# Kernel optimization log

Hardware: AMD Instinct MI355X
Metric: run time of the kernel (lower is better)

The kernel has to match this reference:

```python
import jax, jax.numpy as jnp
import numpy as np

G, NPG, DEG = 64, 1024, 16          # graphs, nodes/graph, avg degree
N, E = G * NPG, G * NPG * DEG        # 65536 nodes, 1048576 edges
F, H = 128, 128                      # num_features, n_hidden
K1, K2 = NPG // 2, NPG // 4          # ceil(0.5*1024)=512, ceil(0.5*512)=256


def setup_inputs() -> dict:
    key = jax.random.key(0)
    ks = jax.random.split(key, 16)
    x = jax.random.normal(ks[0], (N, F), dtype=jnp.float32)
    # edges constrained within each graph (block-diagonal adjacency)
    offs = (jnp.arange(G, dtype=jnp.int32) * NPG)[:, None]
    src = (jax.random.randint(ks[1], (G, E // G), 0, NPG, dtype=jnp.int32) + offs).reshape(-1)
    dst = (jax.random.randint(ks[2], (G, E // G), 0, NPG, dtype=jnp.int32) + offs).reshape(-1)
    def lin(k, fi, fo):
        s = 1.0 / np.sqrt(fi)
        return jax.random.uniform(k, (fi, fo), jnp.float32, -s, s)
    return dict(
        x=x, src=src, dst=dst,
        W1=lin(ks[3], F, H),  b1=jnp.zeros((H,), jnp.float32),
        Ws1=lin(ks[4], H, 1), bs1=jnp.zeros((1,), jnp.float32),
        W2=lin(ks[5], H, H),  b2=jnp.zeros((H,), jnp.float32),
        Ws2=lin(ks[6], H, 1), bs2=jnp.zeros((1,), jnp.float32),
        Wl1=lin(ks[7], 2 * H, H), bl1=jnp.zeros((H,), jnp.float32),
        Wl2=lin(ks[8], H, 1),     bl2=jnp.zeros((1,), jnp.float32),
    )


def gcn_conv(x, src, dst, ew, W, b):
    """GCNConv: D^-1/2 (A+I) D^-1/2 (x W) + b, with edge weights ew."""
    n = x.shape[0]
    h = x @ W
    loop = jnp.arange(n, dtype=src.dtype)
    s = jnp.concatenate([src, loop])
    d = jnp.concatenate([dst, loop])
    w = jnp.concatenate([ew, jnp.ones((n,), x.dtype)])
    deg = jax.ops.segment_sum(w, d, num_segments=n)
    dinv = jnp.where(deg > 0, jax.lax.rsqrt(jnp.maximum(deg, 1e-12)), 0.0)
    norm = dinv[s] * dinv[d] * w
    return jax.ops.segment_sum(norm[:, None] * h[s], d, num_segments=n) + b


def sag_pool(x, src, dst, ew, Ws, bs, n_per_graph, k):
    """SAGPooling: GCN attention score, per-graph top-k, x*tanh(score), edge prune via mask."""
    n = x.shape[0]
    g = n // n_per_graph
    score = gcn_conv(x, src, dst, ew, Ws, bs)[:, 0]                 # [n]
    _, idx = jax.lax.top_k(score.reshape(g, n_per_graph), k)        # [g, k]
    perm = (idx + (jnp.arange(g, dtype=jnp.int32) * n_per_graph)[:, None]).reshape(-1)
    xn = x[perm] * jnp.tanh(score[perm])[:, None]                   # [g*k, H]
    kept = jnp.zeros((n,), bool).at[perm].set(True)
    nmap = jnp.zeros((n,), jnp.int32).at[perm].set(jnp.arange(g * k, dtype=jnp.int32))
    valid = kept[src] & kept[dst] & (ew > 0)
    ewn = jnp.where(valid, ew, 0.0)
    srcn = jnp.where(valid, nmap[src], 0)
    dstn = jnp.where(valid, nmap[dst], 0)
    return xn, srcn, dstn, ewn


def reference(x, src, dst, W1, b1, Ws1, bs1, W2, b2, Ws2, bs2, Wl1, bl1, Wl2, bl2):
    ew = jnp.ones((src.shape[0],), x.dtype)
    h = jax.nn.relu(gcn_conv(x, src, dst, ew, W1, b1))
    h, s1, d1, ew1 = sag_pool(h, src, dst, ew, Ws1, bs1, NPG, K1)
    hb = h.reshape(G, K1, H)
    x1 = jnp.concatenate([hb.max(axis=1), hb.mean(axis=1)], axis=1)  # [G, 2H]
    h = jax.nn.relu(gcn_conv(h, s1, d1, ew1, W2, b2))
    h, s2, d2, ew2 = sag_pool(h, s1, d1, ew1, Ws2, bs2, K1, K2)
    hb = h.reshape(G, K2, H)
    x2 = jnp.concatenate([hb.max(axis=1), hb.mean(axis=1)], axis=1)
    z = x1 + x2
    z = jax.nn.relu(z @ Wl1 + bl1)                                  # dropout: eval mode (identity)
    return (z @ Wl2 + bl2)[:, 0]                                     # [G]
```

## Files before the change

kernel.cpp:

```cpp
#include <hip/hip_runtime.h>
#include <math.h>

constexpr int NN1 = 65536;
constexpr int EE  = 1048576;
constexpr int GG  = 64;
constexpr int HH  = 128;
constexpr int NPG = 1024;
constexpr int EPG = 16384;
constexpr int K1  = 512;
constexpr int M1  = GG * K1;
constexpr int K2  = 256;
constexpr int M2  = GG * K2;

__device__ __forceinline__ int xcd_swz(int bid, int nblk)
{
    return (bid & 7) * (nblk >> 3) + (bid >> 3);
}

__device__ __forceinline__ float4 f4add(float4 a, float4 b)
{
    a.x += b.x; a.y += b.y; a.z += b.z; a.w += b.w; return a;
}

__global__ __launch_bounds__(256) void gemm1_k(const float* __restrict__ A,
                                               const float* __restrict__ W,
                                               const int* __restrict__ rbeg,
                                               const int* __restrict__ rend,
                                               float* __restrict__ C)
{
    __shared__ float Wl[64 * 160];
    const int t    = threadIdx.x;
    const int rowg = t >> 3;
    const int cg   = t & 7;
    const int b    = xcd_swz(blockIdx.x, gridDim.x);
    const int r0   = (b << 7) + rowg;

    const float* Ar0 = A + ((size_t)r0 << 7);
    const float* Ar1 = Ar0 + (32 << 7);
    const float* Ar2 = Ar1 + (32 << 7);
    const float* Ar3 = Ar2 + (32 << 7);

    float acc[4][16];
#pragma unroll
    for (int i = 0; i < 4; ++i)
#pragma unroll
        for (int j = 0; j < 16; ++j) acc[i][j] = 0.f;

    {
        const float4* Wg = (const float4*)W;
#pragma unroll
        for (int i = 0; i < 8; ++i) {
            int idx = t + (i << 8);
            int k   = idx >> 5;
            int c4  = (idx & 31) << 2;
            *(float4*)&Wl[k * 160 + (c4 >> 4) * 20 + (c4 & 15)] = Wg[idx];
        }
    }
    float4 xc0 = *(const float4*)(Ar0), xc1 = *(const float4*)(Ar1);
    float4 xc2 = *(const float4*)(Ar2), xc3 = *(const float4*)(Ar3);
    __syncthreads();

    const float* wbase = &Wl[cg * 20];

#pragma unroll 1
    for (int k0 = 0; k0 < 64; k0 += 4) {
        float4 xn0 = *(const float4*)(Ar0 + k0 + 4);
        float4 xn1 = *(const float4*)(Ar1 + k0 + 4);
        float4 xn2 = *(const float4*)(Ar2 + k0 + 4);
        float4 xn3 = *(const float4*)(Ar3 + k0 + 4);
#pragma unroll
        for (int kk = 0; kk < 4; ++kk) {
            const float* wr = wbase + (k0 + kk) * 160;
            float x0 = ((const float*)&xc0)[kk], x1 = ((const float*)&xc1)[kk];
            float x2 = ((const float*)&xc2)[kk], x3 = ((const float*)&xc3)[kk];
#pragma unroll
            for (int jh = 0; jh < 16; jh += 8) {
                float wv[8];
                *(float4*)&wv[0] = *(const float4*)(wr + jh);
                *(float4*)&wv[4] = *(const float4*)(wr + jh + 4);
#pragma unroll
                for (int j = 0; j < 8; ++j) {
                    acc[0][jh + j] = fmaf(x0, wv[j], acc[0][jh + j]);
                    acc[1][jh + j] = fmaf(x1, wv[j], acc[1][jh + j]);
                    acc[2][jh + j] = fmaf(x2, wv[j], acc[2][jh + j]);
                    acc[3][jh + j] = fmaf(x3, wv[j], acc[3][jh + j]);
                }
            }
        }
        xc0 = xn0; xc1 = xn1; xc2 = xn2; xc3 = xn3;
    }
    __syncthreads();
    {
        const float4* Wg = (const float4*)(W + 64 * 128);
#pragma unroll
        for (int i = 0; i < 8; ++i) {
            int idx = t + (i << 8);
            int k   = idx >> 5;
            int c4  = (idx & 31) << 2;
            *(float4*)&Wl[k * 160 + (c4 >> 4) * 20 + (c4 & 15)] = Wg[idx];
        }
    }
    __syncthreads();

#pragma unroll 1
    for (int k0 = 64; k0 < 128; k0 += 4) {
        bool pf = (k0 < 124);
        float4 xn0, xn1, xn2, xn3;
        if (pf) {
            xn0 = *(const float4*)(Ar0 + k0 + 4);
            xn1 = *(const float4*)(Ar1 + k0 + 4);
            xn2 = *(const float4*)(Ar2 + k0 + 4);
            xn3 = *(const float4*)(Ar3 + k0 + 4);
        }
#pragma unroll
        for (int kk = 0; kk < 4; ++kk) {
            const float* wr = wbase + (k0 - 64 + kk) * 160;
            float x0 = ((const float*)&xc0)[kk], x1 = ((const float*)&xc1)[kk];
            float x2 = ((const float*)&xc2)[kk], x3 = ((const float*)&xc3)[kk];
#pragma unroll
            for (int jh = 0; jh < 16; jh += 8) {
                float wv[8];
                *(float4*)&wv[0] = *(const float4*)(wr + jh);
                *(float4*)&wv[4] = *(const float4*)(wr + jh + 4);
#pragma unroll
                for (int j = 0; j < 8; ++j) {
                    acc[0][jh + j] = fmaf(x0, wv[j], acc[0][jh + j]);
                    acc[1][jh + j] = fmaf(x1, wv[j], acc[1][jh + j]);
                    acc[2][jh + j] = fmaf(x2, wv[j], acc[2][jh + j]);
                    acc[3][jh + j] = fmaf(x3, wv[j], acc[3][jh + j]);
                }
            }
        }
        if (pf) { xc0 = xn0; xc1 = xn1; xc2 = xn2; xc3 = xn3; }
    }

#pragma unroll
    for (int i = 0; i < 4; ++i) {
        int r = r0 + (i << 5);
        float deg = (float)(rend[r] - rbeg[r]) + 1.0f;
        float sc = 1.0f / sqrtf(deg);
        float* cp = C + ((size_t)r << 7) + (cg << 4);
#pragma unroll
        for (int j = 0; j < 16; j += 4) {
            float4 v;
            v.x = acc[i][j] * sc; v.y = acc[i][j + 1] * sc;
            v.z = acc[i][j + 2] * sc; v.w = acc[i][j + 3] * sc;
            *(float4*)(cp + j) = v;
        }
    }
}

__global__ __launch_bounds__(256) void gemm2_k(const float* __restrict__ A,
                                               const float* __restrict__ W,
                                               const int* __restrict__ rbeg,
                                               const int* __restrict__ rend,
                                               const int* __restrict__ perm,
                                               const float* __restrict__ tsel,
                                               float* __restrict__ C)
{
    __shared__ float Wl[64 * 160];
    const int t    = threadIdx.x;
    const int rowg = t >> 3;
    const int cg   = t & 7;
    const int b    = xcd_swz(blockIdx.x, gridDim.x);
    const int r0   = (b << 7) + rowg;

    const float* Ar0 = A + ((size_t)perm[r0] << 7);
    const float* Ar1 = A + ((size_t)perm[r0 + 32] << 7);
    const float* Ar2 = A + ((size_t)perm[r0 + 64] << 7);
    const float* Ar3 = A + ((size_t)perm[r0 + 96] << 7);

    float acc[4][16];
#pragma unroll
    for (int i = 0; i < 4; ++i)
#pragma unroll
        for (int j = 0; j < 16; ++j) acc[i][j] = 0.f;

    {
        const float4* Wg = (const float4*)W;
#pragma unroll
        for (int i = 0; i < 8; ++i) {
            int idx = t + (i << 8);
            int k   = idx >> 5;
            int c4  = (idx & 31) << 2;
            *(float4*)&Wl[k * 160 + (c4 >> 4) * 20 + (c4 & 15)] = Wg[idx];
        }
    }
    float4 xc0 = *(const float4*)(Ar0), xc1 = *(const float4*)(Ar1);
    float4 xc2 = *(const float4*)(Ar2), xc3 = *(const float4*)(Ar3);
    __syncthreads();

    const float* wbase = &Wl[cg * 20];

#pragma unroll 1
    for (int k0 = 0; k0 < 64; k0 += 4) {
        float4 xn0 = *(const float4*)(Ar0 + k0 + 4);
        float4 xn1 = *(const float4*)(Ar1 + k0 + 4);
        float4 xn2 = *(const float4*)(Ar2 + k0 + 4);
        float4 xn3 = *(const float4*)(Ar3 + k0 + 4);
#pragma unroll
        for (int kk = 0; kk < 4; ++kk) {
            const float* wr = wbase + (k0 + kk) * 160;
            float x0 = ((const float*)&xc0)[kk], x1 = ((const float*)&xc1)[kk];
            float x2 = ((const float*)&xc2)[kk], x3 = ((const float*)&xc3)[kk];
#pragma unroll
            for (int jh = 0; jh < 16; jh += 8) {
                float wv[8];
                *(float4*)&wv[0] = *(const float4*)(wr + jh);
                *(float4*)&wv[4] = *(const float4*)(wr + jh + 4);
#pragma unroll
                for (int j = 0; j < 8; ++j) {
                    acc[0][jh + j] = fmaf(x0, wv[j], acc[0][jh + j]);
                    acc[1][jh + j] = fmaf(x1, wv[j], acc[1][jh + j]);
                    acc[2][jh + j] = fmaf(x2, wv[j], acc[2][jh + j]);
                    acc[3][jh + j] = fmaf(x3, wv[j], acc[3][jh + j]);
                }
            }
        }
        xc0 = xn0; xc1 = xn1; xc2 = xn2; xc3 = xn3;
    }
    __syncthreads();
    {
        const float4* Wg = (const float4*)(W + 64 * 128);
#pragma unroll
        for (int i = 0; i < 8; ++i) {
            int idx = t + (i << 8);
            int k   = idx >> 5;
            int c4  = (idx & 31) << 2;
            *(float4*)&Wl[k * 160 + (c4 >> 4) * 20 + (c4 & 15)] = Wg[idx];
        }
    }
    __syncthreads();

#pragma unroll 1
    for (int k0 = 64; k0 < 128; k0 += 4) {
        bool pf = (k0 < 124);
        float4 xn0, xn1, xn2, xn3;
        if (pf) {
            xn0 = *(const float4*)(Ar0 + k0 + 4);
            xn1 = *(const float4*)(Ar1 + k0 + 4);
            xn2 = *(const float4*)(Ar2 + k0 + 4);
            xn3 = *(const float4*)(Ar3 + k0 + 4);
        }
#pragma unroll
        for (int kk = 0; kk < 4; ++kk) {
            const float* wr = wbase + (k0 - 64 + kk) * 160;
            float x0 = ((const float*)&xc0)[kk], x1 = ((const float*)&xc1)[kk];
            float x2 = ((const float*)&xc2)[kk], x3 = ((const float*)&xc3)[kk];
#pragma unroll
            for (int jh = 0; jh < 16; jh += 8) {
                float wv[8];
                *(float4*)&wv[0] = *(const float4*)(wr + jh);
                *(float4*)&wv[4] = *(const float4*)(wr + jh + 4);
#pragma unroll
                for (int j = 0; j < 8; ++j) {
                    acc[0][jh + j] = fmaf(x0, wv[j], acc[0][jh + j]);
                    acc[1][jh + j] = fmaf(x1, wv[j], acc[1][jh + j]);
                    acc[2][jh + j] = fmaf(x2, wv[j], acc[2][jh + j]);
                    acc[3][jh + j] = fmaf(x3, wv[j], acc[3][jh + j]);
                }
            }
        }
        if (pf) { xc0 = xn0; xc1 = xn1; xc2 = xn2; xc3 = xn3; }
    }

#pragma unroll
    for (int i = 0; i < 4; ++i) {
        int r = r0 + (i << 5);
        float deg = (float)(rend[r] - rbeg[r]) + 1.0f;
        float sc = tsel[r] / sqrtf(deg);
        float* cp = C + ((size_t)r << 7) + (cg << 4);
#pragma unroll
        for (int j = 0; j < 16; j += 4) {
            float4 v;
            v.x = acc[i][j] * sc; v.y = acc[i][j + 1] * sc;
            v.z = acc[i][j + 2] * sc; v.w = acc[i][j + 3] * sc;
            *(float4*)(cp + j) = v;
        }
    }
}

__global__ __launch_bounds__(1024) void build_csr1_k(const int* __restrict__ src, const int* __restrict__ dst,
                                                     int* __restrict__ rbeg, int* __restrict__ rend,
                                                     int* __restrict__ csr)
{
    __shared__ int cnt[NPG];
    int t = threadIdx.x;
    int g = xcd_swz(blockIdx.x, GG);
    int ebase = g * EPG;
    cnt[t] = 0;
    __syncthreads();
#pragma unroll
    for (int k = 0; k < EPG / 1024; ++k) {
        int d = dst[ebase + t + k * 1024] & (NPG - 1);
        atomicAdd(&cnt[d], 1);
    }
    __syncthreads();
    int deg0 = cnt[t];
    int val = deg0;
    for (int off = 1; off < NPG; off <<= 1) {
        int u = (t >= off) ? cnt[t - off] : 0;
        __syncthreads();
        val += u; cnt[t] = val;
        __syncthreads();
    }
    int node = g * NPG + t;
    rbeg[node] = ebase + val - deg0;
    rend[node] = ebase + val;
    cnt[t] = val - deg0;
    __syncthreads();
#pragma unroll
    for (int k = 0; k < EPG / 1024; ++k) {
        int e = ebase + t + k * 1024;
        int d = dst[e] & (NPG - 1);
        int pos = atomicAdd(&cnt[d], 1);
        csr[ebase + pos] = src[e];
    }
}

__global__ __launch_bounds__(256) void agg_feat_k(const float4* __restrict__ XWs,
                                                  const int* __restrict__ rbeg, const int* __restrict__ rend,
                                                  const int* __restrict__ csr,
                                                  const float* __restrict__ bias, const float* __restrict__ Ws,
                                                  float* __restrict__ hout, float* __restrict__ hss, int n)
{
    int b    = xcd_swz(blockIdx.x, gridDim.x);
    int half = threadIdx.x >> 5;
    int lane = threadIdx.x & 31;
    int node = (b << 3) + half;
    if (node >= n) return;
    const float4* Xf = XWs + lane;

    float4 A = make_float4(0.f, 0.f, 0.f, 0.f), B = A, C = A, D = A;
    int p0 = rbeg[node], p1 = rend[node];
    int p = p0;
    for (; p + 8 <= p1; p += 8) {
        int s0 = csr[p], s1 = csr[p + 1], s2 = csr[p + 2], s3 = csr[p + 3];
        int s4 = csr[p + 4], s5 = csr[p + 5], s6 = csr[p + 6], s7 = csr[p + 7];
        float4 v0 = Xf[(size_t)s0 << 5], v1 = Xf[(size_t)s1 << 5];
        float4 v2 = Xf[(size_t)s2 << 5], v3 = Xf[(size_t)s3 << 5];
        float4 v4 = Xf[(size_t)s4 << 5], v5 = Xf[(size_t)s5 << 5];
        float4 v6 = Xf[(size_t)s6 << 5], v7 = Xf[(size_t)s7 << 5];
        A = f4add(A, v0); B = f4add(B, v1); C = f4add(C, v2); D = f4add(D, v3);
        A = f4add(A, v4); B = f4add(B, v5); C = f4add(C, v6); D = f4add(D, v7);
    }
    for (; p + 4 <= p1; p += 4) {
        int s0 = csr[p], s1 = csr[p + 1], s2 = csr[p + 2], s3 = csr[p + 3];
        float4 v0 = Xf[(size_t)s0 << 5], v1 = Xf[(size_t)s1 << 5];
        float4 v2 = Xf[(size_t)s2 << 5], v3 = Xf[(size_t)s3 << 5];
        A = f4add(A, v0); B = f4add(B, v1); C = f4add(C, v2); D = f4add(D, v3);
    }
    for (; p < p1; ++p) {
        int s = csr[p];
        A = f4add(A, Xf[(size_t)s << 5]);
    }
    float4 acc = f4add(f4add(A, B), f4add(C, D));
    acc = f4add(acc, Xf[(size_t)node << 5]);

    float dd = 1.0f / sqrtf((float)(p1 - p0) + 1.0f);
    float4 bb = *(const float4*)(bias + (lane << 2));
    acc.x = fmaxf(fmaf(acc.x, dd, bb.x), 0.f);
    acc.y = fmaxf(fmaf(acc.y, dd, bb.y), 0.f);
    acc.z = fmaxf(fmaf(acc.z, dd, bb.z), 0.f);
    acc.w = fmaxf(fmaf(acc.w, dd, bb.w), 0.f);
    *(float4*)(hout + ((size_t)node << 7) + (lane << 2)) = acc;

    float4 wsv = *(const float4*)(Ws + (lane << 2));
    float pq = acc.x * wsv.x + acc.y * wsv.y + acc.z * wsv.z + acc.w * wsv.w;
#pragma unroll
    for (int off = 16; off > 0; off >>= 1) pq += __shfl_down(pq, off, 32);
    if (lane == 0) hss[node] = dd * pq;
}

template <int NNE, int KK, bool BUILD>
__global__ void sctopk_k(const int* __restrict__ rbeg, const int* __restrict__ rend,
                         const int* __restrict__ csr, const float* __restrict__ hss,
                         const float* __restrict__ bsp,
                         int* __restrict__ perm, float* __restrict__ tsel,
                         const int* __restrict__ src, const int* __restrict__ dst,
                         int* __restrict__ rbeg2, int* __restrict__ rend2,
                         int* __restrict__ csr2,
                         const float* __restrict__ h, float* __restrict__ xout)
{
    __shared__ unsigned long long keys[NNE];
    __shared__ float hl[NNE];
    __shared__ int   pix[KK];
    __shared__ float tsl[KK];
    int t = threadIdx.x;
    int g = xcd_swz(blockIdx.x, GG);
    int node = g * NNE + t;
    hl[t] = hss[node];
    __syncthreads();

    int p0 = rbeg[node], p1 = rend[node];
    float a = 0.f, b = 0.f, c = 0.f, e = 0.f;
    int p = p0;
    for (; p + 8 <= p1; p += 8) {
        int s0 = csr[p] & (NNE - 1), s1 = csr[p + 1] & (NNE - 1);
        int s2 = csr[p + 2] & (NNE - 1), s3 = csr[p + 3] & (NNE - 1);
        int s4 = csr[p + 4] & (NNE - 1), s5 = csr[p + 5] & (NNE - 1);
        int s6 = csr[p + 6] & (NNE - 1), s7 = csr[p + 7] & (NNE - 1);
        a += hl[s0]; b += hl[s1]; c += hl[s2]; e += hl[s3];
        a += hl[s4]; b += hl[s5]; c += hl[s6]; e += hl[s7];
    }
    for (; p + 4 <= p1; p += 4) {
        int s0 = csr[p] & (NNE - 1), s1 = csr[p + 1] & (NNE - 1);
        int s2 = csr[p + 2] & (NNE - 1), s3 = csr[p + 3] & (NNE - 1);
        a += hl[s0]; b += hl[s1]; c += hl[s2]; e += hl[s3];
    }
    for (; p < p1; ++p) a += hl[csr[p] & (NNE - 1)];
    float dd = 1.0f / sqrtf((float)(p1 - p0) + 1.0f);
    float s = fmaf((a + b) + (c + e) + hl[t], dd, bsp[0]);

    unsigned u = __float_as_uint(s);
    u = (u & 0x80000000u) ? ~u : (u | 0x80000000u);
    __syncthreads();
    keys[t] = (((unsigned long long)u) << 32) | (unsigned)(NNE - 1 - t);
    __syncthreads();
    for (int k = 2; k <= NNE; k <<= 1) {
        for (int j = k >> 1; j > 0; j >>= 1) {
            int ixj = t ^ j;
            if (ixj > t) {
                unsigned long long ka = keys[t], kb = keys[ixj];
                bool up = ((t & k) == 0);
                if ((ka > kb) == up) { keys[t] = kb; keys[ixj] = ka; }
            }
            __syncthreads();
        }
    }
    unsigned long long key = keys[NNE - 1 - t];
    int idx = NNE - 1 - (int)(key & 0xFFFFFFFFu);
    if (t < KK) {
        unsigned uu = (unsigned)(key >> 32);
        float sc = __uint_as_float((uu & 0x80000000u) ? (uu ^ 0x80000000u) : ~uu);
        float tv = tanhf(sc);
        pix[t] = g * NNE + idx;
        tsl[t] = tv;
        if (BUILD) {
            perm[g * KK + t] = g * NNE + idx;
            tsel[g * KK + t] = tv;
        }
    }

    if (BUILD) {
        constexpr int EPT = BUILD ? (EPG / NNE) : 1;
        __syncthreads();
        int* nml = (int*)hl;
        int* cnt = (int*)keys;
        nml[t] = -1;
        if (t < KK) cnt[t] = 0;
        __syncthreads();
        if (t < KK) nml[idx] = t;
        __syncthreads();

        int ebase = g * EPG;
        int nsl[EPT], ndl[EPT];
#pragma unroll
        for (int k = 0; k < EPT; ++k) {
            int e = ebase + t + k * NNE;
            nsl[k] = nml[src[e] & (NNE - 1)];
            ndl[k] = nml[dst[e] & (NNE - 1)];
            if (nsl[k] >= 0 && ndl[k] >= 0) atomicAdd(&cnt[ndl[k]], 1);
        }
        __syncthreads();
        int deg0 = 0, val = 0;
        if (t < KK) { deg0 = cnt[t]; val = deg0; }
        for (int off = 1; off < KK; off <<= 1) {
            int u2 = (t < KK && t >= off) ? cnt[t - off] : 0;
            __syncthreads();
            if (t < KK) { val += u2; cnt[t] = val; }
            __syncthreads();
        }
        if (t < KK) {
            int n2 = g * KK + t;
            rbeg2[n2] = ebase + val - deg0;
            rend2[n2] = ebase + val;
            cnt[t] = val - deg0;
        }
        __syncthreads();
#pragma unroll
        for (int k = 0; k < EPT; ++k) {
            if (nsl[k] >= 0 && ndl[k] >= 0) {
                int pos = atomicAdd(&cnt[ndl[k]], 1);
                csr2[ebase + pos] = g * KK + nsl[k];
            }
        }
    }

    constexpr int G = NNE / 128;
    __syncthreads();
    float* rmax = (float*)keys;
    float* rsum = rmax + G * 128;
    int col = t & 127;
    int grp = t >> 7;
    float mx = -INFINITY, sm = 0.f;
#pragma unroll 8
    for (int rr0 = 0; rr0 < KK / G; ++rr0) {
        int rr = grp + rr0 * G;
        int o = pix[rr];
        float tv = tsl[rr];
        float v = h[((size_t)o << 7) + col] * tv;
        mx = fmaxf(mx, v);
        sm += v;
    }
    rmax[grp * 128 + col] = mx;
    rsum[grp * 128 + col] = sm;
    __syncthreads();
    if (t < 128) {
        float m = rmax[t], s2 = rsum[t];
#pragma unroll
        for (int j2 = 1; j2 < G; ++j2) {
            m = fmaxf(m, rmax[j2 * 128 + t]);
            s2 += rsum[j2 * 128 + t];
        }
        xout[g * 256 + t] = m;
        xout[g * 256 + 128 + t] = s2 * (1.0f / (float)KK);
    }
}

__global__ __launch_bounds__(128) void mlp_k(const float* __restrict__ x1, const float* __restrict__ x2,
                                             const float* __restrict__ Wl1, const float* __restrict__ bl1,
                                             const float* __restrict__ Wl2, const float* __restrict__ bl2,
                                             float* __restrict__ out)
{
    __shared__ float z[256];
    __shared__ float red[128];
    int g = blockIdx.x, t = threadIdx.x;
    z[t]       = x1[g * 256 + t]       + x2[g * 256 + t];
    z[t + 128] = x1[g * 256 + 128 + t] + x2[g * 256 + 128 + t];
    __syncthreads();
    float acc = bl1[t];
    for (int k = 0; k < 256; ++k) acc = fmaf(z[k], Wl1[k * 128 + t], acc);
    float zz = fmaxf(acc, 0.f);
    red[t] = zz * Wl2[t];
    __syncthreads();
    for (int off = 64; off > 0; off >>= 1) {
        if (t < off) red[t] += red[t + off];
        __syncthreads();
    }
    if (t == 0) out[g] = red[0] + bl2[0];
}

extern "C" void kernel_launch(void* const* d_in, const int* in_sizes, int n_in,
                              void* d_out, int out_size, void* d_ws, size_t ws_size,
                              hipStream_t stream)
{
    const float* x   = (const float*)d_in[0];
    const int*   src = (const int*)d_in[1];
    const int*   dst = (const int*)d_in[2];
    const float* W1  = (const float*)d_in[3];
    const float* b1  = (const float*)d_in[4];
    const float* Ws1 = (const float*)d_in[5];
    const float* bs1 = (const float*)d_in[6];
    const float* W2  = (const float*)d_in[7];
    const float* b2  = (const float*)d_in[8];
    const float* Ws2 = (const float*)d_in[9];
    const float* bs2 = (const float*)d_in[10];
    const float* Wl1 = (const float*)d_in[11];
    const float* bl1 = (const float*)d_in[12];
    const float* Wl2 = (const float*)d_in[13];
    const float* bl2 = (const float*)d_in[14];
    float* out = (float*)d_out;
    char* ws = (char*)d_ws;

    float* XW1 = (float*)(ws);
    float* h1  = (float*)(ws + ((size_t)32 << 20));
    float* XW2 = (float*)(ws);
    float* h2  = (float*)(ws + ((size_t)16 << 20));
    size_t SB = (size_t)64 << 20;
    auto alloc = [&](size_t bytes) { char* p = ws + SB; SB += (bytes + 255) & ~(size_t)255; return p; };
    int* csr1     = (int*)alloc((size_t)EE * 4);
    int* rbeg1    = (int*)alloc(NN1 * 4);
    int* rend1    = (int*)alloc(NN1 * 4);
    float* hss1   = (float*)alloc(NN1 * 4);
    int* perm1    = (int*)alloc(M1 * 4);
    float* tsel1  = (float*)alloc(M1 * 4);
    int* rbeg2    = (int*)alloc(M1 * 4);
    int* rend2    = (int*)alloc(M1 * 4);
    float* hss2   = (float*)alloc(M1 * 4);
    float* x1b    = (float*)alloc(GG * 256 * 4);
    float* x2b    = (float*)alloc(GG * 256 * 4);
    int* csr2     = csr1;
    (void)ws_size; (void)in_sizes; (void)n_in; (void)out_size;

    build_csr1_k<<<GG, 1024, 0, stream>>>(src, dst, rbeg1, rend1, csr1);
    gemm1_k<<<NN1 / 128, 256, 0, stream>>>(x, W1, rbeg1, rend1, XW1);
    agg_feat_k<<<NN1 / 8, 256, 0, stream>>>((const float4*)XW1, rbeg1, rend1, csr1, b1, Ws1, h1, hss1, NN1);
    sctopk_k<NPG, K1, true><<<GG, NPG, 0, stream>>>(rbeg1, rend1, csr1, hss1, bs1, perm1, tsel1,
                                                    src, dst, rbeg2, rend2, csr2, h1, x1b);
    gemm2_k<<<M1 / 128, 256, 0, stream>>>(h1, W2, rbeg2, rend2, perm1, tsel1, XW2);
    agg_feat_k<<<M1 / 8, 256, 0, stream>>>((const float4*)XW2, rbeg2, rend2, csr2, b2, Ws2, h2, hss2, M1);
    sctopk_k<K1, K2, false><<<GG, K1, 0, stream>>>(rbeg2, rend2, csr2, hss2, bs2, nullptr, nullptr,
                                                   nullptr, nullptr, nullptr, nullptr, nullptr, h2, x2b);
    mlp_k<<<GG, 128, 0, stream>>>(x1b, x2b, Wl1, bl1, Wl2, bl2, out);
}
```

Measured before the change: 186.9 us.

## Build pooled CSR from existing CSR rows and fuse MLP head into second top-k

The pooled-graph CSR is now built by having each kept node walk its own incoming CSR row and count or emit surviving sources, instead of rescanning the raw src/dst edge lists with shared-memory atomics. This removes the global edge-list reads and atomic position allocation, but produces per-thread serial loops over variable-length rows. The final MLP is fused into the second top-k kernel, which drops one launch and the x2 round trip through global memory. csr2 gets its own buffer because the row walk reads csr1 while writing.

New measurement: 187.8 us. No clear change (+0.5%).

```diff
diff --git a/kernel.cpp b/kernel.cpp
--- a/kernel.cpp
+++ b/kernel.cpp
@@ -372,23 +372,29 @@
     if (lane == 0) hss[node] = dd * pq;
 }
 
-template <int NNE, int KK, bool BUILD>
+template <int NNE, int KK, bool BUILD, bool HEAD>
 __global__ void sctopk_k(const int* __restrict__ rbeg, const int* __restrict__ rend,
                          const int* __restrict__ csr, const float* __restrict__ hss,
                          const float* __restrict__ bsp,
                          int* __restrict__ perm, float* __restrict__ tsel,
-                         const int* __restrict__ src, const int* __restrict__ dst,
                          int* __restrict__ rbeg2, int* __restrict__ rend2,
                          int* __restrict__ csr2,
-                         const float* __restrict__ h, float* __restrict__ xout)
+                         const float* __restrict__ h, float* __restrict__ xout,
+                         const float* __restrict__ x1g,
+                         const float* __restrict__ Wl1, const float* __restrict__ bl1,
+                         const float* __restrict__ Wl2, const float* __restrict__ bl2,
+                         float* __restrict__ outp)
 {
     __shared__ unsigned long long keys[NNE];
     __shared__ float hl[NNE];
     __shared__ int   pix[KK];
     __shared__ float tsl[KK];
+    __shared__ float zm[256];
+    __shared__ float red[128];
     int t = threadIdx.x;
     int g = xcd_swz(blockIdx.x, GG);
     int node = g * NNE + t;
+    int ebase = g * EPG;
     hl[t] = hss[node];
     __syncthreads();
 
@@ -443,24 +449,20 @@
     }
 
     if (BUILD) {
-        constexpr int EPT = BUILD ? (EPG / NNE) : 1;
         __syncthreads();
         int* nml = (int*)hl;
         int* cnt = (int*)keys;
         nml[t] = -1;
-        if (t < KK) cnt[t] = 0;
         __syncthreads();
         if (t < KK) nml[idx] = t;
         __syncthreads();
 
-        int ebase = g * EPG;
-        int nsl[EPT], ndl[EPT];
-#pragma unroll
-        for (int k = 0; k < EPT; ++k) {
-            int e = ebase + t + k * NNE;
-            nsl[k] = nml[src[e] & (NNE - 1)];
-            ndl[k] = nml[dst[e] & (NNE - 1)];
-            if (nsl[k] >= 0 && ndl[k] >= 0) atomicAdd(&cnt[ndl[k]], 1);
+        int myrank = nml[t];
+        int deg2 = 0;
+        if (myrank >= 0) {
+            for (int q = p0; q < p1; ++q)
+                if (nml[csr[q] & (NNE - 1)] >= 0) ++deg2;
+            cnt[myrank] = deg2;
         }
         __syncthreads();
         int deg0 = 0, val = 0;
@@ -478,11 +480,11 @@
             cnt[t] = val - deg0;
         }
         __syncthreads();
-#pragma unroll
-        for (int k = 0; k < EPT; ++k) {
-            if (nsl[k] >= 0 && ndl[k] >= 0) {
-                int pos = atomicAdd(&cnt[ndl[k]], 1);
-                csr2[ebase + pos] = g * KK + nsl[k];
+        if (myrank >= 0) {
+            int pos = ebase + cnt[myrank];
+            for (int q = p0; q < p1; ++q) {
+                int sl = nml[csr[q] & (NNE - 1)];
+                if (sl >= 0) csr2[pos++] = g * KK + sl;
             }
         }
     }
@@ -506,39 +508,41 @@
     rmax[grp * 128 + col] = mx;
     rsum[grp * 128 + col] = sm;
     __syncthreads();
-    if (t < 128) {
-        float m = rmax[t], s2 = rsum[t];
-#pragma unroll
-        for (int j2 = 1; j2 < G; ++j2) {
-            m = fmaxf(m, rmax[j2 * 128 + t]);
-            s2 += rsum[j2 * 128 + t];
-        }
-        xout[g * 256 + t] = m;
-        xout[g * 256 + 128 + t] = s2 * (1.0f / (float)KK);
-    }
-}
-
-__global__ __launch_bounds__(128) void mlp_k(const float* __restrict__ x1, const float* __restrict__ x2,
-                                             const float* __restrict__ Wl1, const float* __restrict__ bl1,
-                                             const float* __restrict__ Wl2, const float* __restrict__ bl2,
-                                             float* __restrict__ out)
-{
-    __shared__ float z[256];
-    __shared__ float red[128];
-    int g = blockIdx.x, t = threadIdx.x;
-    z[t]       = x1[g * 256 + t]       + x2[g * 256 + t];
-    z[t + 128] = x1[g * 256 + 128 + t] + x2[g * 256 + 128 + t];
-    __syncthreads();
-    float acc = bl1[t];
-    for (int k = 0; k < 256; ++k) acc = fmaf(z[k], Wl1[k * 128 + t], acc);
-    float zz = fmaxf(acc, 0.f);
-    red[t] = zz * Wl2[t];
-    __syncthreads();
-    for (int off = 64; off > 0; off >>= 1) {
-        if (t < off) red[t] += red[t + off];
-        __syncthreads();
-    }
-    if (t == 0) out[g] = red[0] + bl2[0];
+    if (!HEAD) {
+        if (t < 128) {
+            float m = rmax[t], s2 = rsum[t];
+#pragma unroll
+            for (int j2 = 1; j2 < G; ++j2) {
+                m = fmaxf(m, rmax[j2 * 128 + t]);
+                s2 += rsum[j2 * 128 + t];
+            }
+            xout[g * 256 + t] = m;
+            xout[g * 256 + 128 + t] = s2 * (1.0f / (float)KK);
+        }
+    } else {
+        if (t < 128) {
+            float m = rmax[t], s2 = rsum[t];
+#pragma unroll
+            for (int j2 = 1; j2 < G; ++j2) {
+                m = fmaxf(m, rmax[j2 * 128 + t]);
+                s2 += rsum[j2 * 128 + t];
+            }
+            zm[t]       = x1g[g * 256 + t]       + m;
+            zm[t + 128] = x1g[g * 256 + 128 + t] + s2 * (1.0f / (float)KK);
+        }
+        __syncthreads();
+        if (t < 128) {
+            float acc = bl1[t];
+            for (int k = 0; k < 256; ++k) acc = fmaf(zm[k], Wl1[k * 128 + t], acc);
+            red[t] = fmaxf(acc, 0.f) * Wl2[t];
+        }
+        __syncthreads();
+        for (int off = 64; off > 0; off >>= 1) {
+            if (t < off) red[t] += red[t + off];
+            __syncthreads();
+        }
+        if (t == 0) outp[g] = red[0] + bl2[0];
+    }
 }
 
 extern "C" void kernel_launch(void* const* d_in, const int* in_sizes, int n_in,
@@ -570,6 +574,7 @@
     size_t SB = (size_t)64 << 20;
     auto alloc = [&](size_t bytes) { char* p = ws + SB; SB += (bytes + 255) & ~(size_t)255; return p; };
     int* csr1     = (int*)alloc((size_t)EE * 4);
+    int* csr2     = (int*)alloc((size_t)EE * 4);
     int* rbeg1    = (int*)alloc(NN1 * 4);
     int* rend1    = (int*)alloc(NN1 * 4);
     float* hss1   = (float*)alloc(NN1 * 4);
@@ -579,18 +584,17 @@
     int* rend2    = (int*)alloc(M1 * 4);
     float* hss2   = (float*)alloc(M1 * 4);
     float* x1b    = (float*)alloc(GG * 256 * 4);
-    float* x2b    = (float*)alloc(GG * 256 * 4);
-    int* csr2     = csr1;
     (void)ws_size; (void)in_sizes; (void)n_in; (void)out_size;
 
     build_csr1_k<<<GG, 1024, 0, stream>>>(src, dst, rbeg1, rend1, csr1);
     gemm1_k<<<NN1 / 128, 256, 0, stream>>>(x, W1, rbeg1, rend1, XW1);
     agg_feat_k<<<NN1 / 8, 256, 0, stream>>>((const float4*)XW1, rbeg1, rend1, csr1, b1, Ws1, h1, hss1, NN1);
-    sctopk_k<NPG, K1, true><<<GG, NPG, 0, stream>>>(rbeg1, rend1, csr1, hss1, bs1, perm1, tsel1,
-                                                    src, dst, rbeg2, rend2, csr2, h1, x1b);
+    sctopk_k<NPG, K1, true, false><<<GG, NPG, 0, stream>>>(rbeg1, rend1, csr1, hss1, bs1, perm1, tsel1,
+                                                           rbeg2, rend2, csr2, h1, x1b,
+                                                           nullptr, nullptr, nullptr, nullptr, nullptr, nullptr);
     gemm2_k<<<M1 / 128, 256, 0, stream>>>(h1, W2, rbeg2, rend2, perm1, tsel1, XW2);
     agg_feat_k<<<M1 / 8, 256, 0, stream>>>((const float4*)XW2, rbeg2, rend2, csr2, b2, Ws2, h2, hss2, M1);
-    sctopk_k<K1, K2, false><<<GG, K1, 0, stream>>>(rbeg2, rend2, csr2, hss2, bs2, nullptr, nullptr,
-                                                   nullptr, nullptr, nullptr, nullptr, nullptr, h2, x2b);
-    mlp_k<<<GG, 128, 0, stream>>>(x1b, x2b, Wl1, bl1, Wl2, bl2, out);
-}
+    sctopk_k<K1, K2, false, true><<<GG, K1, 0, stream>>>(rbeg2, rend2, csr2, hss2, bs2, nullptr, nullptr,
+                                                         nullptr, nullptr, nullptr, h2, nullptr,
+                                                         x1b, Wl1, bl1, Wl2, bl2, out);
+}
```
